# Kernel optimization log

Measured on AMD Instinct MI355X. Metric: run time of the kernel, lower is better.

Reference implementation:

```python
import jax, jax.numpy as jnp
import numpy as np

# static config (matches init_kwargs)
H = 64; W = 64; WS = 8; SHIFT = 4; HEADS = 16; DIM = 512; TED = 512; B = 16
NW = (H // WS) * (W // WS)          # 64 windows
WS2 = WS * WS                        # 64 tokens per window
N = WS2 + 1                          # +1 time-embedding token appended per window
HIDDEN = int(DIM * 4.0)


def _rel_pos_index():
    # standard Swin relative-position index over the WS*WS window tokens
    coords = np.stack(np.meshgrid(np.arange(WS), np.arange(WS), indexing='ij'))  # (2, WS, WS)
    cf = coords.reshape(2, -1)
    rel = (cf[:, :, None] - cf[:, None, :]).transpose(1, 2, 0)  # (WS2, WS2, 2)
    rel[..., 0] += WS - 1
    rel[..., 1] += WS - 1
    rel[..., 0] *= 2 * WS - 1
    return rel.sum(-1)  # (WS2, WS2) int


def _attn_mask():
    # shifted-window attention mask, exactly as built in __init__
    img_mask = np.zeros((H, W), dtype=np.float32)
    slices = (slice(0, -WS), slice(-WS, -SHIFT), slice(-SHIFT, None))
    cnt = 0
    for hs in slices:
        for ws_ in slices:
            img_mask[hs, ws_] = cnt
            cnt += 1
    mw = img_mask.reshape(H // WS, WS, W // WS, WS).transpose(0, 2, 1, 3).reshape(-1, WS2)  # (NW, WS2)
    diff = mw[:, None, :] - mw[:, :, None]
    return np.where(diff != 0, -100.0, 0.0).astype(np.float32)  # (NW, WS2, WS2)


def _ln(x, g, b):
    m = x.mean(-1, keepdims=True)
    v = ((x - m) ** 2).mean(-1, keepdims=True)
    return (x - m) / jnp.sqrt(v + 1e-5) * g + b


def setup_inputs() -> dict:
    key = jax.random.key(0)
    ks = jax.random.split(key, 10)
    s = 0.02
    return {
        'x': jax.random.normal(ks[0], (B, H * W, DIM), dtype=jnp.float32),
        'emb': jax.random.normal(ks[1], (B, TED), dtype=jnp.float32),
        'gamma1': jnp.ones((DIM,), jnp.float32),
        'beta1': jnp.zeros((DIM,), jnp.float32),
        'W_emb': jax.random.normal(ks[2], (TED, DIM), jnp.float32) * s,
        'b_emb': jnp.zeros((DIM,), jnp.float32),
        'W_qkv': jax.random.normal(ks[3], (DIM, 3 * DIM), jnp.float32) * s,
        'b_qkv': jnp.zeros((3 * DIM,), jnp.float32),
        'rel_bias_table': jax.random.normal(ks[4], ((2 * WS - 1) ** 2, HEADS), jnp.float32) * s,
        'W_proj': jax.random.normal(ks[5], (DIM, DIM), jnp.float32) * s,
        'b_proj': jnp.zeros((DIM,), jnp.float32),
        'gamma2': jnp.ones((DIM,), jnp.float32),
        'beta2': jnp.zeros((DIM,), jnp.float32),
        'W1': jax.random.normal(ks[6], (DIM, HIDDEN), jnp.float32) * s,
        'b1': jnp.zeros((HIDDEN,), jnp.float32),
        'W2': jax.random.normal(ks[7], (HIDDEN, DIM), jnp.float32) * s,
        'b2': jnp.zeros((DIM,), jnp.float32),
    }


def reference(x, emb, gamma1, beta1, W_emb, b_emb, W_qkv, b_qkv, rel_bias_table,
              W_proj, b_proj, gamma2, beta2, W1, b1, W2, b2):
    Bb, L, C = x.shape
    hd = C // HEADS
    shortcut = x
    # norm1 -> spatial -> cyclic shift
    xn = _ln(x, gamma1, beta1).reshape(Bb, H, W, C)
    xs = jnp.roll(xn, (-SHIFT, -SHIFT), axis=(1, 2))
    # window partition: (B, NW, WS2, C)
    xw = xs.reshape(Bb, H // WS, WS, W // WS, WS, C).transpose(0, 1, 3, 2, 4, 5)
    xw = xw.reshape(Bb, NW, WS2, C)
    # append time-embedding token to each window
    t = jax.nn.silu(emb) @ W_emb + b_emb                       # (B, C)
    t = jnp.broadcast_to(t[:, None, None, :], (Bb, NW, 1, C))
    xw = jnp.concatenate([xw, t], axis=2).reshape(Bb * NW, N, C)
    # windowed multi-head attention
    qkv = (xw @ W_qkv + b_qkv).reshape(Bb * NW, N, 3, HEADS, hd).transpose(2, 0, 3, 1, 4)
    q, k, v = qkv[0] * (hd ** -0.5), qkv[1], qkv[2]            # (B*NW, HEADS, N, hd)
    attn = jnp.einsum('bhnd,bhmd->bhnm', q, k)
    bias = rel_bias_table[_rel_pos_index().reshape(-1)].reshape(WS2, WS2, HEADS).transpose(2, 0, 1)
    bias = jnp.pad(bias, ((0, 0), (0, 1), (0, 1)))             # zero bias for time token
    attn = attn + bias[None]
    mask = jnp.pad(jnp.asarray(_attn_mask()), ((0, 0), (0, 1), (0, 1)))  # (NW, N, N)
    attn = attn.reshape(Bb, NW, HEADS, N, N) + mask[None, :, None]
    attn = jax.nn.softmax(attn.reshape(Bb * NW, HEADS, N, N), axis=-1)
    out = jnp.einsum('bhnm,bhmd->bnhd', attn, v).reshape(Bb * NW, N, C)
    out = (out @ W_proj + b_proj)[:, :WS2]                     # drop time token
    # window reverse + reverse shift
    out = out.reshape(Bb, H // WS, W // WS, WS, WS, C).transpose(0, 1, 3, 2, 4, 5).reshape(Bb, H, W, C)
    out = jnp.roll(out, (SHIFT, SHIFT), axis=(1, 2)).reshape(Bb, L, C)
    x1 = shortcut + out
    # norm2 + MLP (exact GELU, as torch nn.GELU default)
    hmid = jax.nn.gelu(_ln(x1, gamma2, beta2) @ W1 + b1, approximate=False)
    return x1 + hmid @ W2 + b2
```

## Files before the change

kernel.cpp:

```cpp
#include <hip/hip_runtime.h>
#include <hip/hip_bf16.h>

typedef __hip_bfloat16 bf16;
typedef short short4_t __attribute__((ext_vector_type(4)));
typedef short short8 __attribute__((ext_vector_type(8)));
typedef float f32x4 __attribute__((ext_vector_type(4)));

#define DIMC 512
#define HEADS_ 16
#define NTOK 65
#define NWIN 64
#define NB 16
#define HID 2048
#define TOTROWS 66560
#define ATT_CHUNK_WB 128
#define ATT_CHUNK_ROWS (ATT_CHUNK_WB * NTOK)
#define MLP_CHUNK_ROWS 16384


__device__ __forceinline__ float b2f(short s) {
  unsigned int u = ((unsigned int)(unsigned short)s) << 16;
  float f; __builtin_memcpy(&f, &u, 4); return f;
}
__device__ __forceinline__ short f2s(float f) {
  bf16 b = __float2bfloat16(f);
  short s; __builtin_memcpy(&s, &b, 2); return s;
}

__device__ __forceinline__ void async_lds16(const bf16* g, bf16* l) {
  __builtin_amdgcn_global_load_lds(
      (const __attribute__((address_space(1))) unsigned int*)g,
      (__attribute__((address_space(3))) unsigned int*)l,
      16, 0, 0);
}

__device__ __forceinline__ void wave_stats512(const float* v, float& m, float& rstd)
{
  float s = 0.0f, ss = 0.0f;
  #pragma unroll
  for (int e = 0; e < 8; ++e) { s += v[e]; ss += v[e] * v[e]; }
  #pragma unroll
  for (int o = 1; o < 64; o <<= 1) { s += __shfl_xor(s, o); ss += __shfl_xor(ss, o); }
  m = s * (1.0f / 512.0f);
  rstd = rsqrtf(ss * (1.0f / 512.0f) - m * m + 1e-5f);
}


__global__ __launch_bounds__(256) void time_emb_kernel(
    const float* __restrict__ emb, const float* __restrict__ W_emb,
    const float* __restrict__ b_emb, float* __restrict__ t)
{
  int b = blockIdx.x;
  int c = blockIdx.y * 256 + threadIdx.x;
  __shared__ float se[512];
  for (int k = threadIdx.x; k < 512; k += 256) {
    float e = emb[b * 512 + k];
    se[k] = e / (1.0f + expf(-e));
  }
  __syncthreads();
  float acc = b_emb[c];
  for (int k = 0; k < 512; ++k) acc += se[k] * W_emb[k * 512 + c];
  t[b * 512 + c] = acc;
}

__global__ void transpose_cast_kernel(const float* __restrict__ W, bf16* __restrict__ Wt,
                                      int Kd, int Nd)
{
  __shared__ float tile[32][33];
  int n0 = blockIdx.x * 32, k0 = blockIdx.y * 32;
  for (int r = threadIdx.y; r < 32; r += 8)
    tile[r][threadIdx.x] = W[(long)(k0 + r) * Nd + n0 + threadIdx.x];
  __syncthreads();
  for (int r = threadIdx.y; r < 32; r += 8)
    Wt[(long)(n0 + r) * Kd + k0 + threadIdx.x] = __float2bfloat16(tile[threadIdx.x][r]);
}

__global__ __launch_bounds__(256) void bias_mask_kernel(
    const float* __restrict__ btab, float* __restrict__ tbl)
{
  int h = blockIdx.x, wt = blockIdx.y;
  for (int idx = threadIdx.x; idx < 6400; idx += 256) {
    int i = idx / 80, t = idx % 80;
    float v;
    if (t >= 65) v = -1e30f;
    else if (i >= 64 || t == 64) v = 0.0f;
    else {
      int rel = (((i >> 3) - (t >> 3) + 7) * 15) + ((i & 7) - (t & 7) + 7);
      v = btab[rel * HEADS_ + h];
      int rci = (wt & 2) ? (((i >> 3) < 4) ? 1 : 2) : 0;
      int cci = (wt & 1) ? (((i & 7) < 4) ? 1 : 2) : 0;
      int rct = (wt & 2) ? (((t >> 3) < 4) ? 1 : 2) : 0;
      int cct = (wt & 1) ? (((t & 7) < 4) ? 1 : 2) : 0;
      if (rci * 3 + cci != rct * 3 + cct) v -= 100.0f;
    }
    tbl[(h * 4 + wt) * 6400 + idx] = v;
  }
}

__global__ __launch_bounds__(256) void ln1_window_kernel(
    const float* __restrict__ x, const float* __restrict__ gamma,
    const float* __restrict__ beta, const float* __restrict__ t,
    bf16* __restrict__ xw)
{
  long r = (long)blockIdx.x * 4 + (threadIdx.x >> 6);
  int lane = threadIdx.x & 63;
  int wb = (int)(r / NTOK), i = (int)(r % NTOK);
  int b = wb >> 6, w = wb & 63;
  bf16* out = xw + r * 512 + lane * 8;
  if (i == 64) {
    const float* tr = t + b * 512 + lane * 8;
    short8 o;
    #pragma unroll
    for (int e = 0; e < 8; ++e) o[e] = f2s(tr[e]);
    *(short8*)out = o;
    return;
  }
  int wh = w >> 3, ww = w & 7, ih = i >> 3, iw = i & 7;
  int hsrc = ((wh * 8 + ih) + 4) & 63;
  int wsrc = ((ww * 8 + iw) + 4) & 63;
  const float* xr = x + ((long)b * 4096 + hsrc * 64 + wsrc) * 512 + lane * 8;
  float v[8];
  *(f32x4*)&v[0] = *(const f32x4*)xr;
  *(f32x4*)&v[4] = *(const f32x4*)(xr + 4);
  float m, rstd;
  wave_stats512(v, m, rstd);
  const float* g = gamma + lane * 8;
  const float* bt = beta + lane * 8;
  short8 o;
  #pragma unroll
  for (int e = 0; e < 8; ++e) o[e] = f2s((v[e] - m) * rstd * g[e] + bt[e]);
  *(short8*)out = o;
}

__global__ __launch_bounds__(256) void ln2_kernel(
    const float* __restrict__ x1, const float* __restrict__ gamma,
    const float* __restrict__ beta, bf16* __restrict__ out)
{
  long r = (long)blockIdx.x * 4 + (threadIdx.x >> 6);
  int lane = threadIdx.x & 63;
  const float* xr = x1 + r * 512 + lane * 8;
  float v[8];
  *(f32x4*)&v[0] = *(const f32x4*)xr;
  *(f32x4*)&v[4] = *(const f32x4*)(xr + 4);
  float m, rstd;
  wave_stats512(v, m, rstd);
  const float* g = gamma + lane * 8;
  const float* bt = beta + lane * 8;
  short8 o;
  #pragma unroll
  for (int e = 0; e < 8; ++e) o[e] = f2s((v[e] - m) * rstd * g[e] + bt[e]);
  *(short8*)(out + r * 512 + lane * 8) = o;
}

template<int EPI>
__global__ __launch_bounds__(512, 2) void gemm8_kernel(
    const bf16* __restrict__ A, const bf16* __restrict__ Bt,
    const float* __restrict__ bias, int N, int K,
    bf16* __restrict__ outB, float* __restrict__ outF,
    const float* __restrict__ xin, int rowOffset)
{
  __shared__ bf16 lds[2][2][256 * 64];
  const int tid = threadIdx.x;
  const int lane = tid & 63;
  const int wv = tid >> 6;
  const int wm = wv >> 2, wn = wv & 3;
  const int fr = lane & 15, fg = lane >> 4;
  const long row0 = (long)blockIdx.y * 256;
  const long col0 = (long)blockIdx.x * 256;

  const int srow = lane >> 3;
  const int sslot = (lane & 7) ^ srow;
  const int c0 = wv * 2;

  f32x4 acc[8][4] = {};
  const int nkt = K >> 6;

  auto stage_tile = [&](int buf, int gk) {
    #pragma unroll
    for (int q2 = 0; q2 < 2; ++q2) {
      int rr = (c0 + q2) * 8;
      const bf16* pA = A + (row0 + rr + srow) * (long)K + gk + sslot * 8;
      const bf16* pB = Bt + (col0 + rr + srow) * (long)K + gk + sslot * 8;
      bf16* dA = &lds[buf][0][rr * 64];
      bf16* dB = &lds[buf][1][rr * 64];
      async_lds16(pA, dA);
      async_lds16(pA + (long)128 * K, dA + 128 * 64);
      async_lds16(pB, dB);
      async_lds16(pB + (long)128 * K, dB + 128 * 64);
    }
  };
  auto frag = [&](const bf16* tile, int row, int slotB) -> short8 {
    return *(const short8*)((const char*)tile + row * 128 + ((slotB ^ (row & 7)) << 4));
  };

  stage_tile(0, 0);
  asm volatile("s_waitcnt vmcnt(0)" ::: "memory");
  asm volatile("s_barrier" ::: "memory");

  for (int i = 0; i < nkt; ++i) {
    const bf16* At = &lds[i & 1][0][0];
    const bf16* Bl = &lds[i & 1][1][0];
    const bool st = (i + 1 < nkt);
    short8 breg[4][2];
    #pragma unroll
    for (int ph = 0; ph < 4; ++ph) {
      short8 a[2][2];
      #pragma unroll
      for (int m2 = 0; m2 < 2; ++m2)
        #pragma unroll
        for (int ks = 0; ks < 2; ++ks)
          a[m2][ks] = frag(At, wm * 128 + (ph * 2 + m2) * 16 + fr, ks * 4 + fg);
      if (ph == 0) {
        #pragma unroll
        for (int ni = 0; ni < 4; ++ni)
          #pragma unroll
          for (int ks = 0; ks < 2; ++ks)
            breg[ni][ks] = frag(Bl, wn * 64 + ni * 16 + fr, ks * 4 + fg);
        if (st) stage_tile((i & 1) ^ 1, (i + 1) << 6);
      }
      asm volatile("s_barrier" ::: "memory");
      __builtin_amdgcn_s_setprio(1);
      #pragma unroll
      for (int m2 = 0; m2 < 2; ++m2)
        #pragma unroll
        for (int ni = 0; ni < 4; ++ni)
          #pragma unroll
          for (int ks = 0; ks < 2; ++ks)
            acc[ph * 2 + m2][ni] = __builtin_amdgcn_mfma_f32_16x16x32_bf16(
                a[m2][ks], breg[ni][ks], acc[ph * 2 + m2][ni], 0, 0, 0);
      __builtin_amdgcn_s_setprio(0);
      if (ph == 3 && st) asm volatile("s_waitcnt vmcnt(0)" ::: "memory");
      asm volatile("s_barrier" ::: "memory");
    }
  }

  float bs[4];
  #pragma unroll
  for (int ni = 0; ni < 4; ++ni) bs[ni] = bias[col0 + wn * 64 + ni * 16 + fr];
  #pragma unroll
  for (int mi = 0; mi < 8; ++mi) {
    #pragma unroll
    for (int j = 0; j < 4; ++j) {
      long rr = row0 + wm * 128 + mi * 16 + fg * 4 + j;
      if (EPI == 2) {
        int grow = rowOffset + (int)rr;
        int ii = grow % NTOK;
        if (ii == 64) continue;
        int wb = grow / NTOK;
        int b = wb >> 6, w = wb & 63;
        int wh = w >> 3, ww = w & 7, ih = ii >> 3, iw = ii & 7;
        int hh   = ((wh * 8 + ih) + 4) & 63;
        int wcol = ((ww * 8 + iw) + 4) & 63;
        long orow = ((long)b * 4096 + hh * 64 + wcol) * 512;
        #pragma unroll
        for (int ni = 0; ni < 4; ++ni) {
          long o = orow + col0 + wn * 64 + ni * 16 + fr;
          outF[o] = xin[o] + acc[mi][ni][j] + bs[ni];
        }
      } else {
        #pragma unroll
        for (int ni = 0; ni < 4; ++ni) {
          long cc = col0 + wn * 64 + ni * 16 + fr;
          float v = acc[mi][ni][j] + bs[ni];
          if (EPI == 0) {
            outB[rr * N + cc] = __float2bfloat16(v);
          } else if (EPI == 1) {
            float g = 0.5f * v * (1.0f + erff(v * 0.70710678118654752f));
            outB[rr * N + cc] = __float2bfloat16(g);
          } else {
            long o = rr * N + cc;
            outF[o] = outF[o] + v;
          }
        }
      }
    }
  }
}

__global__ __launch_bounds__(64, 2) void attn_mfma_kernel(
    const bf16* __restrict__ qkv, bf16* __restrict__ attnO,
    const float* __restrict__ tbl, int wb0)
{
  __shared__ bf16 P[80 * 104];
  const int lwb = blockIdx.x, h = blockIdx.y;
  const int lane = threadIdx.x;
  const int fr = lane & 15, g = lane >> 4;
  const float scale = 0.17677669529663687f;
  const bf16* base = qkv + (long)lwb * 65 * 1536 + h * 32 + g * 8;

  for (int idx = lane; idx < 240; idx += 64) {
    int i = idx / 3, s = idx % 3;
    *(short8*)&P[i * 104 + 80 + s * 8] = (short8){0, 0, 0, 0, 0, 0, 0, 0};
  }

  short8 bq[5];
  #pragma unroll
  for (int tn = 0; tn < 5; ++tn) {
    int qr = tn * 16 + fr; qr = qr > 64 ? 64 : qr;
    bq[tn] = *(const short8*)(base + (long)qr * 1536);
  }

  f32x4 acc[5][5];
  #pragma unroll
  for (int tm = 0; tm < 5; ++tm) {
    int kr = tm * 16 + fr; kr = kr > 64 ? 64 : kr;
    short8 ak = *(const short8*)(base + 512 + (long)kr * 1536);
    #pragma unroll
    for (int tn = 0; tn < 5; ++tn)
      acc[tm][tn] = __builtin_amdgcn_mfma_f32_16x16x32_bf16(
          ak, bq[tn], (f32x4){0.0f, 0.0f, 0.0f, 0.0f}, 0, 0, 0);
  }

  const int w = (wb0 + lwb) & 63;
  const int wt = (((w >> 3) == 7) ? 2 : 0) + (((w & 7) == 7) ? 1 : 0);
  const float* tp = tbl + (h * 4 + wt) * 6400;
  #pragma unroll
  for (int tn = 0; tn < 5; ++tn) {
    const int i = tn * 16 + fr;
    const float* ti = tp + i * 80 + g * 4;
    float m = -3.0e38f;
    #pragma unroll
    for (int tm = 0; tm < 5; ++tm) {
      f32x4 bv = *(const f32x4*)(ti + tm * 16);
      #pragma unroll
      for (int r = 0; r < 4; ++r) {
        float s = fmaf(acc[tm][tn][r], scale, bv[r]);
        acc[tm][tn][r] = s;
        m = fmaxf(m, s);
      }
    }
    m = fmaxf(m, __shfl_xor(m, 16));
    m = fmaxf(m, __shfl_xor(m, 32));
    float l = 0.0f;
    #pragma unroll
    for (int tm = 0; tm < 5; ++tm)
      #pragma unroll
      for (int r = 0; r < 4; ++r) {
        float e = __expf(acc[tm][tn][r] - m);
        acc[tm][tn][r] = e;
        l += e;
      }
    l += __shfl_xor(l, 16);
    l += __shfl_xor(l, 32);
    float inv = 1.0f / l;
    #pragma unroll
    for (int tm = 0; tm < 5; ++tm) {
      short4_t pk;
      #pragma unroll
      for (int r = 0; r < 4; ++r) pk[r] = f2s(acc[tm][tn][r] * inv);
      *(short4_t*)&P[i * 104 + tm * 16 + g * 4] = pk;
    }
  }

  const bf16* vbase = qkv + (long)lwb * 65 * 1536 + 1024 + h * 32;
  f32x4 oacc[2][5] = {};
  #pragma unroll
  for (int kt = 0; kt < 3; ++kt) {
    short8 bp[5];
    #pragma unroll
    for (int tn = 0; tn < 5; ++tn)
      bp[tn] = *(const short8*)&P[(tn * 16 + fr) * 104 + kt * 32 + g * 8];
    #pragma unroll
    for (int ma = 0; ma < 2; ++ma) {
      short8 av;
      #pragma unroll
      for (int e = 0; e < 8; ++e) {
        int vr = kt * 32 + g * 8 + e; vr = vr > 64 ? 64 : vr;
        av[e] = *(const short*)(vbase + (long)vr * 1536 + ma * 16 + fr);
      }
      #pragma unroll
      for (int tn = 0; tn < 5; ++tn)
        oacc[ma][tn] = __builtin_amdgcn_mfma_f32_16x16x32_bf16(
            av, bp[tn], oacc[ma][tn], 0, 0, 0);
    }
  }

  #pragma unroll
  for (int tn = 0; tn < 5; ++tn) {
    int i = tn * 16 + fr;
    if (i < 65) {
      bf16* op = attnO + (long)(lwb * 65 + i) * 512 + h * 32 + g * 4;
      #pragma unroll
      for (int ma = 0; ma < 2; ++ma) {
        short4_t o4;
        #pragma unroll
        for (int r = 0; r < 4; ++r) o4[r] = f2s(oacc[ma][tn][r]);
        *(short4_t*)(op + ma * 16) = o4;
      }
    }
  }
}


extern "C" void kernel_launch(void* const* d_in, const int* in_sizes, int n_in,
                              void* d_out, int out_size, void* d_ws, size_t ws_size,
                              hipStream_t stream)
{
  const float* x      = (const float*)d_in[0];
  const float* emb    = (const float*)d_in[1];
  const float* gamma1 = (const float*)d_in[2];
  const float* beta1  = (const float*)d_in[3];
  const float* W_emb  = (const float*)d_in[4];
  const float* b_emb  = (const float*)d_in[5];
  const float* W_qkv  = (const float*)d_in[6];
  const float* b_qkv  = (const float*)d_in[7];
  const float* btab   = (const float*)d_in[8];
  const float* W_proj = (const float*)d_in[9];
  const float* b_proj = (const float*)d_in[10];
  const float* gamma2 = (const float*)d_in[11];
  const float* beta2  = (const float*)d_in[12];
  const float* W1     = (const float*)d_in[13];
  const float* b1     = (const float*)d_in[14];
  const float* W2     = (const float*)d_in[15];
  const float* b2     = (const float*)d_in[16];
  float* out = (float*)d_out;
  (void)n_in; (void)in_sizes; (void)out_size;

  char* ws = (char*)d_ws;
  size_t off = 0;
  auto alloc = [&](size_t bytes) -> char* {
    char* p = ws + off;
    off += (bytes + 255) & ~(size_t)255;
    return p;
  };
  bf16* wt_qkv  = (bf16*)alloc((size_t)1536 * 512 * 2);
  bf16* wt_proj = (bf16*)alloc((size_t)512 * 512 * 2);
  bf16* wt1     = (bf16*)alloc((size_t)2048 * 512 * 2);
  bf16* wt2     = (bf16*)alloc((size_t)512 * 2048 * 2);
  float* tvec   = (float*)alloc((size_t)16 * 512 * 4);
  float* tbl    = (float*)alloc((size_t)16 * 4 * 6400 * 4);

  const size_t sz_xw    = (size_t)TOTROWS * 512 * 2;
  const size_t sz_qkv   = (size_t)TOTROWS * 1536 * 2;
  const size_t sz_attnO = (size_t)TOTROWS * 512 * 2;
  const bool big = ws_size >= off + sz_xw + sz_qkv + sz_attnO + (4u << 20);

  transpose_cast_kernel<<<dim3(1536 / 32, 512 / 32), dim3(32, 8), 0, stream>>>(W_qkv, wt_qkv, 512, 1536);
  transpose_cast_kernel<<<dim3(512 / 32, 512 / 32),  dim3(32, 8), 0, stream>>>(W_proj, wt_proj, 512, 512);
  transpose_cast_kernel<<<dim3(2048 / 32, 512 / 32), dim3(32, 8), 0, stream>>>(W1, wt1, 512, 2048);
  transpose_cast_kernel<<<dim3(512 / 32, 2048 / 32), dim3(32, 8), 0, stream>>>(W2, wt2, 2048, 512);
  time_emb_kernel<<<dim3(16, 2), 256, 0, stream>>>(emb, W_emb, b_emb, tvec);
  bias_mask_kernel<<<dim3(16, 4), 256, 0, stream>>>(btab, tbl);

  if (big) {
    bf16* xw    = (bf16*)alloc(sz_xw);
    bf16* qkv   = (bf16*)alloc(sz_qkv);
    bf16* attnO = (bf16*)alloc(sz_attnO);
    bf16* ln2b  = xw;
    bf16* h     = qkv;

    ln1_window_kernel<<<TOTROWS / 4, 256, 0, stream>>>(x, gamma1, beta1, tvec, xw);
    gemm8_kernel<0><<<dim3(6, 260), 512, 0, stream>>>(
        xw, wt_qkv, b_qkv, 1536, 512, qkv, nullptr, nullptr, 0);
    attn_mfma_kernel<<<dim3(NB * NWIN, HEADS_), 64, 0, stream>>>(qkv, attnO, tbl, 0);
    gemm8_kernel<2><<<dim3(2, 260), 512, 0, stream>>>(
        attnO, wt_proj, b_proj, 512, 512, nullptr, out, x, 0);
    ln2_kernel<<<65536 / 4, 256, 0, stream>>>(out, gamma2, beta2, ln2b);
    gemm8_kernel<1><<<dim3(8, 256), 512, 0, stream>>>(
        ln2b, wt1, b1, 2048, 512, h, nullptr, nullptr, 0);
    gemm8_kernel<3><<<dim3(2, 256), 512, 0, stream>>>(
        h, wt2, b2, 512, 2048, nullptr, out, nullptr, 0);
  } else {
    char* regionA = alloc(sz_xw);
    bf16* xw   = (bf16*)regionA;
    bf16* ln2b = (bf16*)regionA;
    bf16* qkv_c = (bf16*)alloc((size_t)8448 * 1536 * 2);
    char* regionB = alloc(sz_attnO);
    bf16* attnO = (bf16*)regionB;
    bf16* h_c   = (bf16*)regionB;

    ln1_window_kernel<<<TOTROWS / 4, 256, 0, stream>>>(x, gamma1, beta1, tvec, xw);
    for (int ac = 0; ac < 8; ++ac) {
      long r0 = (long)ac * ATT_CHUNK_ROWS;
      gemm8_kernel<0><<<dim3(6, 33), 512, 0, stream>>>(
          xw + r0 * 512, wt_qkv, b_qkv, 1536, 512, qkv_c, nullptr, nullptr, 0);
      attn_mfma_kernel<<<dim3(ATT_CHUNK_WB, HEADS_), 64, 0, stream>>>(
          qkv_c, attnO + r0 * 512, tbl, ac * ATT_CHUNK_WB);
    }
    gemm8_kernel<2><<<dim3(2, 260), 512, 0, stream>>>(
        attnO, wt_proj, b_proj, 512, 512, nullptr, out, x, 0);
    ln2_kernel<<<65536 / 4, 256, 0, stream>>>(out, gamma2, beta2, ln2b);
    for (int mc = 0; mc < 4; ++mc) {
      long r0 = (long)mc * MLP_CHUNK_ROWS;
      gemm8_kernel<1><<<dim3(8, 64), 512, 0, stream>>>(
          ln2b + r0 * 512, wt1, b1, 2048, 512, h_c, nullptr, nullptr, 0);
      gemm8_kernel<3><<<dim3(2, 64), 512, 0, stream>>>(
          h_c, wt2, b2, 512, 2048, nullptr, out + r0 * 512, nullptr, 0);
    }
  }
}
```

Baseline: 943.0 us.

## Replace GEMM with 128x256 tile, K=32 stages, XCD-aware block remap, tanh GELU

Rewrites the GEMM kernel to use 128x256 output tiles with 32-wide K stages and smaller LDS buffers. This lets four 512-thread blocks share a CU and simplifies the barrier structure. A 1D grid is remapped so that consecutive tiles land on the same XCD, which should improve L2 reuse. The exact erf GELU becomes a tanh approximation using exp. That changes numerics slightly, and halving K per stage means more barriers per unit of work.

```diff
diff --git a/kernel.cpp b/kernel.cpp
--- a/kernel.cpp
+++ b/kernel.cpp
@@ -15,7 +15,6 @@
 #define TOTROWS 66560
 #define ATT_CHUNK_WB 128
 #define ATT_CHUNK_ROWS (ATT_CHUNK_WB * NTOK)
-#define MLP_CHUNK_ROWS 16384
 
 
 __device__ __forceinline__ float b2f(short s) {
@@ -43,6 +42,15 @@
   for (int o = 1; o < 64; o <<= 1) { s += __shfl_xor(s, o); ss += __shfl_xor(ss, o); }
   m = s * (1.0f / 512.0f);
   rstd = rsqrtf(ss * (1.0f / 512.0f) - m * m + 1e-5f);
+}
+
+__device__ __forceinline__ float gelu_t(float v) {
+  float u = v + 0.044715f * v * v * v;
+  float z2 = 1.5957691216f * fabsf(u);
+  float t = __expf(-z2);
+  float th = 1.0f - 2.0f * t / (1.0f + t);
+  th = (u < 0.0f) ? -th : th;
+  return 0.5f * v * (1.0f + th);
 }
 
 
@@ -153,95 +161,73 @@
 }
 
 template<int EPI>
-__global__ __launch_bounds__(512, 2) void gemm8_kernel(
+__global__ __launch_bounds__(512, 4) void gemmk_kernel(
     const bf16* __restrict__ A, const bf16* __restrict__ Bt,
-    const float* __restrict__ bias, int N, int K,
+    const float* __restrict__ bias, int N, int K, int nx,
     bf16* __restrict__ outB, float* __restrict__ outF,
     const float* __restrict__ xin, int rowOffset)
 {
-  __shared__ bf16 lds[2][2][256 * 64];
+  __shared__ bf16 lA[2][128 * 32];
+  __shared__ bf16 lB[2][256 * 32];
   const int tid = threadIdx.x;
-  const int lane = tid & 63;
-  const int wv = tid >> 6;
+  const int lane = tid & 63, wv = tid >> 6;
   const int wm = wv >> 2, wn = wv & 3;
   const int fr = lane & 15, fg = lane >> 4;
-  const long row0 = (long)blockIdx.y * 256;
-  const long col0 = (long)blockIdx.x * 256;
-
-  const int srow = lane >> 3;
-  const int sslot = (lane & 7) ^ srow;
-  const int c0 = wv * 2;
-
-  f32x4 acc[8][4] = {};
-  const int nkt = K >> 6;
-
-  auto stage_tile = [&](int buf, int gk) {
-    #pragma unroll
-    for (int q2 = 0; q2 < 2; ++q2) {
-      int rr = (c0 + q2) * 8;
-      const bf16* pA = A + (row0 + rr + srow) * (long)K + gk + sslot * 8;
-      const bf16* pB = Bt + (col0 + rr + srow) * (long)K + gk + sslot * 8;
-      bf16* dA = &lds[buf][0][rr * 64];
-      bf16* dB = &lds[buf][1][rr * 64];
-      async_lds16(pA, dA);
-      async_lds16(pA + (long)128 * K, dA + 128 * 64);
-      async_lds16(pB, dB);
-      async_lds16(pB + (long)128 * K, dB + 128 * 64);
-    }
+
+  const int nwg = gridDim.x, bid = blockIdx.x;
+  const int q = nwg >> 3, rr8 = nwg & 7;
+  const int xcd = bid & 7, idx = bid >> 3;
+  const int sid = (xcd < rr8 ? xcd * (q + 1) : rr8 * (q + 1) + (xcd - rr8) * q) + idx;
+  const long row0 = (long)(sid / nx) * 128;
+  const long col0 = (long)(sid % nx) * 256;
+
+  const int rl = lane >> 2, sp = lane & 3;
+  const int s = sp ^ ((rl >> 1) & 3);
+  const bf16* gA  = A  + (row0 + wv * 16 + rl) * (long)K + s * 8;
+  const bf16* gB0 = Bt + (col0 + wv * 16 + rl) * (long)K + s * 8;
+  const bf16* gB1 = Bt + (col0 + 128 + wv * 16 + rl) * (long)K + s * 8;
+
+  f32x4 acc[4][4] = {};
+  const int nkt = K >> 5;
+  const int swr = (fg ^ ((fr >> 1) & 3)) << 4;
+
+  auto stage = [&](int buf, int kt) {
+    async_lds16(gA + kt, &lA[buf][wv * 512]);
+    async_lds16(gB0 + kt, &lB[buf][wv * 512]);
+    async_lds16(gB1 + kt, &lB[buf][4096 + wv * 512]);
   };
-  auto frag = [&](const bf16* tile, int row, int slotB) -> short8 {
-    return *(const short8*)((const char*)tile + row * 128 + ((slotB ^ (row & 7)) << 4));
-  };
-
-  stage_tile(0, 0);
-  asm volatile("s_waitcnt vmcnt(0)" ::: "memory");
-  asm volatile("s_barrier" ::: "memory");
-
-  for (int i = 0; i < nkt; ++i) {
-    const bf16* At = &lds[i & 1][0][0];
-    const bf16* Bl = &lds[i & 1][1][0];
-    const bool st = (i + 1 < nkt);
-    short8 breg[4][2];
-    #pragma unroll
-    for (int ph = 0; ph < 4; ++ph) {
-      short8 a[2][2];
-      #pragma unroll
-      for (int m2 = 0; m2 < 2; ++m2)
-        #pragma unroll
-        for (int ks = 0; ks < 2; ++ks)
-          a[m2][ks] = frag(At, wm * 128 + (ph * 2 + m2) * 16 + fr, ks * 4 + fg);
-      if (ph == 0) {
-        #pragma unroll
-        for (int ni = 0; ni < 4; ++ni)
-          #pragma unroll
-          for (int ks = 0; ks < 2; ++ks)
-            breg[ni][ks] = frag(Bl, wn * 64 + ni * 16 + fr, ks * 4 + fg);
-        if (st) stage_tile((i & 1) ^ 1, (i + 1) << 6);
-      }
-      asm volatile("s_barrier" ::: "memory");
-      __builtin_amdgcn_s_setprio(1);
-      #pragma unroll
-      for (int m2 = 0; m2 < 2; ++m2)
-        #pragma unroll
-        for (int ni = 0; ni < 4; ++ni)
-          #pragma unroll
-          for (int ks = 0; ks < 2; ++ks)
-            acc[ph * 2 + m2][ni] = __builtin_amdgcn_mfma_f32_16x16x32_bf16(
-                a[m2][ks], breg[ni][ks], acc[ph * 2 + m2][ni], 0, 0, 0);
-      __builtin_amdgcn_s_setprio(0);
-      if (ph == 3 && st) asm volatile("s_waitcnt vmcnt(0)" ::: "memory");
-      asm volatile("s_barrier" ::: "memory");
-    }
+
+  stage(0, 0);
+  __syncthreads();
+
+  for (int t = 0; t < nkt; ++t) {
+    const int buf = t & 1;
+    if (t + 1 < nkt) stage(buf ^ 1, (t + 1) << 5);
+    short8 af[4], bfv[4];
+    #pragma unroll
+    for (int mi = 0; mi < 4; ++mi)
+      af[mi] = *(const short8*)((const char*)&lA[buf][0] + (wm * 64 + mi * 16 + fr) * 64 + swr);
+    #pragma unroll
+    for (int ni = 0; ni < 4; ++ni)
+      bfv[ni] = *(const short8*)((const char*)&lB[buf][0] + (wn * 64 + ni * 16 + fr) * 64 + swr);
+    __builtin_amdgcn_s_setprio(1);
+    #pragma unroll
+    for (int mi = 0; mi < 4; ++mi)
+      #pragma unroll
+      for (int ni = 0; ni < 4; ++ni)
+        acc[mi][ni] = __builtin_amdgcn_mfma_f32_16x16x32_bf16(af[mi], bfv[ni], acc[mi][ni], 0, 0, 0);
+    __builtin_amdgcn_s_setprio(0);
+    __syncthreads();
   }
 
   float bs[4];
   #pragma unroll
   for (int ni = 0; ni < 4; ++ni) bs[ni] = bias[col0 + wn * 64 + ni * 16 + fr];
   #pragma unroll
-  for (int mi = 0; mi < 8; ++mi) {
+  for (int mi = 0; mi < 4; ++mi) {
     #pragma unroll
     for (int j = 0; j < 4; ++j) {
-      long rr = row0 + wm * 128 + mi * 16 + fg * 4 + j;
+      long rr = row0 + wm * 64 + mi * 16 + fg * 4 + j;
       if (EPI == 2) {
         int grow = rowOffset + (int)rr;
         int ii = grow % NTOK;
@@ -265,8 +251,7 @@
           if (EPI == 0) {
             outB[rr * N + cc] = __float2bfloat16(v);
           } else if (EPI == 1) {
-            float g = 0.5f * v * (1.0f + erff(v * 0.70710678118654752f));
-            outB[rr * N + cc] = __float2bfloat16(g);
+            outB[rr * N + cc] = __float2bfloat16(gelu_t(v));
           } else {
             long o = rr * N + cc;
             outF[o] = outF[o] + v;
@@ -289,8 +274,8 @@
   const bf16* base = qkv + (long)lwb * 65 * 1536 + h * 32 + g * 8;
 
   for (int idx = lane; idx < 240; idx += 64) {
-    int i = idx / 3, s = idx % 3;
-    *(short8*)&P[i * 104 + 80 + s * 8] = (short8){0, 0, 0, 0, 0, 0, 0, 0};
+    int i = idx / 3, sl = idx % 3;
+    *(short8*)&P[i * 104 + 80 + sl * 8] = (short8){0, 0, 0, 0, 0, 0, 0, 0};
   }
 
   short8 bq[5];
@@ -324,9 +309,9 @@
       f32x4 bv = *(const f32x4*)(ti + tm * 16);
       #pragma unroll
       for (int r = 0; r < 4; ++r) {
-        float s = fmaf(acc[tm][tn][r], scale, bv[r]);
-        acc[tm][tn][r] = s;
-        m = fmaxf(m, s);
+        float sv = fmaf(acc[tm][tn][r], scale, bv[r]);
+        acc[tm][tn][r] = sv;
+        m = fmaxf(m, sv);
       }
     }
     m = fmaxf(m, __shfl_xor(m, 16));
@@ -450,21 +435,21 @@
     bf16* h     = qkv;
 
     ln1_window_kernel<<<TOTROWS / 4, 256, 0, stream>>>(x, gamma1, beta1, tvec, xw);
-    gemm8_kernel<0><<<dim3(6, 260), 512, 0, stream>>>(
-        xw, wt_qkv, b_qkv, 1536, 512, qkv, nullptr, nullptr, 0);
+    gemmk_kernel<0><<<6 * 520, 512, 0, stream>>>(
+        xw, wt_qkv, b_qkv, 1536, 512, 6, qkv, nullptr, nullptr, 0);
     attn_mfma_kernel<<<dim3(NB * NWIN, HEADS_), 64, 0, stream>>>(qkv, attnO, tbl, 0);
-    gemm8_kernel<2><<<dim3(2, 260), 512, 0, stream>>>(
-        attnO, wt_proj, b_proj, 512, 512, nullptr, out, x, 0);
+    gemmk_kernel<2><<<2 * 520, 512, 0, stream>>>(
+        attnO, wt_proj, b_proj, 512, 512, 2, nullptr, out, x, 0);
     ln2_kernel<<<65536 / 4, 256, 0, stream>>>(out, gamma2, beta2, ln2b);
-    gemm8_kernel<1><<<dim3(8, 256), 512, 0, stream>>>(
-        ln2b, wt1, b1, 2048, 512, h, nullptr, nullptr, 0);
-    gemm8_kernel<3><<<dim3(2, 256), 512, 0, stream>>>(
-        h, wt2, b2, 512, 2048, nullptr, out, nullptr, 0);
+    gemmk_kernel<1><<<8 * 512, 512, 0, stream>>>(
+        ln2b, wt1, b1, 2048, 512, 8, h, nullptr, nullptr, 0);
+    gemmk_kernel<3><<<2 * 512, 512, 0, stream>>>(
+        h, wt2, b2, 512, 2048, 2, nullptr, out, nullptr, 0);
   } else {
     char* regionA = alloc(sz_xw);
     bf16* xw   = (bf16*)regionA;
     bf16* ln2b = (bf16*)regionA;
-    bf16* qkv_c = (bf16*)alloc((size_t)8448 * 1536 * 2);
+    bf16* qkv_c = (bf16*)alloc((size_t)ATT_CHUNK_ROWS * 1536 * 2);
     char* regionB = alloc(sz_attnO);
     bf16* attnO = (bf16*)regionB;
     bf16* h_c   = (bf16*)regionB;
@@ -472,20 +457,20 @@
     ln1_window_kernel<<<TOTROWS / 4, 256, 0, stream>>>(x, gamma1, beta1, tvec, xw);
     for (int ac = 0; ac < 8; ++ac) {
       long r0 = (long)ac * ATT_CHUNK_ROWS;
-      gemm8_kernel<0><<<dim3(6, 33), 512, 0, stream>>>(
-          xw + r0 * 512, wt_qkv, b_qkv, 1536, 512, qkv_c, nullptr, nullptr, 0);
+      gemmk_kernel<0><<<6 * 65, 512, 0, stream>>>(
+          xw + r0 * 512, wt_qkv, b_qkv, 1536, 512, 6, qkv_c, nullptr, nullptr, 0);
       attn_mfma_kernel<<<dim3(ATT_CHUNK_WB, HEADS_), 64, 0, stream>>>(
           qkv_c, attnO + r0 * 512, tbl, ac * ATT_CHUNK_WB);
     }
-    gemm8_kernel<2><<<dim3(2, 260), 512, 0, stream>>>(
-        attnO, wt_proj, b_proj, 512, 512, nullptr, out, x, 0);
+    gemmk_kernel<2><<<2 * 520, 512, 0, stream>>>(
+        attnO, wt_proj, b_proj, 512, 512, 2, nullptr, out, x, 0);
     ln2_kernel<<<65536 / 4, 256, 0, stream>>>(out, gamma2, beta2, ln2b);
     for (int mc = 0; mc < 4; ++mc) {
-      long r0 = (long)mc * MLP_CHUNK_ROWS;
-      gemm8_kernel<1><<<dim3(8, 64), 512, 0, stream>>>(
-          ln2b + r0 * 512, wt1, b1, 2048, 512, h_c, nullptr, nullptr, 0);
-      gemm8_kernel<3><<<dim3(2, 64), 512, 0, stream>>>(
-          h_c, wt2, b2, 512, 2048, nullptr, out + r0 * 512, nullptr, 0);
-    }
-  }
-}
+      long r0 = (long)mc * 16384;
+      gemmk_kernel<1><<<8 * 128, 512, 0, stream>>>(
+          ln2b + r0 * 512, wt1, b1, 2048, 512, 8, h_c, nullptr, nullptr, 0);
+      gemmk_kernel<3><<<2 * 128, 512, 0, stream>>>(
+          h_c, wt2, b2, 512, 2048, 2, nullptr, out + r0 * 512, nullptr, 0);
+    }
+  }
+}
```

Result: faster. 896.3 us (-5.0%).
